# Optimization experiments

Measured on AMD Instinct MI355X. Metric: run time of the kernel, lower is better.

Reference implementation:

```python
import jax, jax.numpy as jnp
import numpy as np

N, F, S, D = 8, 16, 196, 1024
H = 8
HD = D // H
L = 1 + F * S  # global feature token + f*s patch tokens


def _ln(x, g, b, eps=1e-5):
    m = x.mean(-1, keepdims=True)
    v = ((x - m) ** 2).mean(-1, keepdims=True)
    return (x - m) / jnp.sqrt(v + eps) * g + b


def _attn(q, k, v, hd):
    s = jnp.einsum('bqd,bkd->bqk', q, k) / jnp.sqrt(jnp.asarray(hd, q.dtype))
    return jnp.einsum('bqk,bkd->bqd', jax.nn.softmax(s, axis=-1), v)


def setup_inputs() -> dict:
    key = jax.random.key(0)
    ks = jax.random.split(key, 8)
    sc = 0.02
    return {
        'x': jax.random.normal(ks[0], (N, L, D), jnp.float32),
        'W_in': jax.random.normal(ks[1], (D, D), jnp.float32) * sc,
        'b_in': jnp.zeros((D,), jnp.float32),
        'g_in': jnp.ones((D,), jnp.float32),
        'beta_in': jnp.zeros((D,), jnp.float32),
        'W_q': jax.random.normal(ks[2], (D, D), jnp.float32) * sc,
        'W_k': jax.random.normal(ks[3], (D, D), jnp.float32) * sc,
        'W_v': jax.random.normal(ks[4], (D, D), jnp.float32) * sc,
        'g_out': jnp.ones((D,), jnp.float32),
        'beta_out': jnp.zeros((D,), jnp.float32),
        'W_out': jax.random.normal(ks[5], (D, D), jnp.float32) * sc,
        'b_out': jnp.zeros((D,), jnp.float32),
        'att_type': 1,  # 1 == 'time', 0 == 'space' (static)
    }


def reference(x, W_in, b_in, g_in, beta_in, W_q, W_k, W_v, g_out, beta_out, W_out, b_out, att_type):
    n = x.shape[0]
    nh = n * H
    # in_fc: Linear + LayerNorm
    x = _ln(x @ W_in + b_in, g_in, beta_in)
    q, k, v = x @ W_q, x @ W_k, x @ W_v

    def split_heads(y):  # [n, L, D] -> [n*h, L, hd]
        return y.reshape(n, L, H, HD).transpose(0, 2, 1, 3).reshape(nh, L, HD)

    q, k, v = map(split_heads, (q, k, v))
    feat_q, q = q[:, :1], q[:, 1:]
    feat_k, k = k[:, :1], k[:, 1:]
    feat_v, v = v[:, :1], v[:, 1:]

    # token_att is computed in the original but never used (dead code):
    # token_att = _attn(feat_q, k, v, HD)

    if att_type == 1:  # time attention: windows of length F per spatial site
        qt = q.reshape(nh, F, S, HD).transpose(0, 2, 1, 3).reshape(nh * S, F, HD)
        kt = k.reshape(nh, F, S, HD).transpose(0, 2, 1, 3).reshape(nh * S, F, HD)
        vt = v.reshape(nh, F, S, HD).transpose(0, 2, 1, 3).reshape(nh * S, F, HD)
        fk = jnp.tile(feat_k, (S, 1, 1))  # torch .repeat(s,1,1)
        fv = jnp.tile(feat_v, (S, 1, 1))
        kk = jnp.concatenate((fk, kt), axis=1)  # [nh*s, 1+f, hd]
        vv = jnp.concatenate((fv, vt), axis=1)
        seq = _attn(qt, kk, vv, HD)  # [nh*s, f, hd]
        seq = seq.reshape(nh, S, F, HD).transpose(0, 2, 1, 3).reshape(nh, F * S, HD)
    else:  # space attention: windows of length S per frame
        qs = q.reshape(nh * F, S, HD)
        ks_ = k.reshape(nh * F, S, HD)
        vs = v.reshape(nh * F, S, HD)
        fk = jnp.tile(feat_k, (F, 1, 1))
        fv = jnp.tile(feat_v, (F, 1, 1))
        kk = jnp.concatenate((fk, ks_), axis=1)  # [nh*f, 1+s, hd]
        vv = jnp.concatenate((fv, vs), axis=1)
        seq = _attn(qs, kk, vv, HD)  # [nh*f, s, hd]
        seq = seq.reshape(nh, F * S, HD)

    out = jnp.concatenate((feat_q, seq), axis=1)  # [nh, L, hd]
    out = out.reshape(n, H, L, HD).transpose(0, 2, 1, 3).reshape(n, L, D)
    out = _ln(out, g_out, beta_out) @ W_out + b_out
    return out
```

## Files before the change

### kernel.cpp

```cpp
#include <hip/hip_runtime.h>
#include <stdint.h>

#define N_B 8
#define F_T 16
#define S_T 196
#define D_M 1024
#define H_N 8
#define HD  128
#define L_T 3137
#define M_R (N_B * L_T)
#define M_P 25216

typedef __attribute__((ext_vector_type(8))) short bf16x8;
typedef __attribute__((ext_vector_type(4))) float f32x4;

__device__ __forceinline__ float b2f(unsigned int u) {
  union { unsigned int i; float f; } x; x.i = u << 16; return x.f;
}
__device__ __forceinline__ unsigned short f2b(float f) {
  union { float f; unsigned int i; } x; x.f = f;
  unsigned int r = x.i + 0x7fffu + ((x.i >> 16) & 1u);
  return (unsigned short)(r >> 16);
}

__global__ __launch_bounds__(256) void convert_pad(const float* __restrict__ x,
                                                   unsigned short* __restrict__ xb,
                                                   int nreal) {
  int i = (blockIdx.x * 256 + threadIdx.x) * 4;
  float4 v;
  if (i < nreal) v = *(const float4*)(x + i);
  else { v.x = 0.f; v.y = 0.f; v.z = 0.f; v.w = 0.f; }
  ushort4 o;
  o.x = f2b(v.x); o.y = f2b(v.y); o.z = f2b(v.z); o.w = f2b(v.w);
  *(ushort4*)(xb + i) = o;
}

struct WP { const float* s[5]; unsigned short* d[5]; };
__global__ __launch_bounds__(256) void transpose5(WP p) {
  __shared__ float t[32][33];
  const int w = blockIdx.z;
  const float* W = p.s[w];
  unsigned short* Wt = p.d[w];
  const int tx = threadIdx.x, ty = threadIdx.y;
  const int n0 = blockIdx.x * 32, k0 = blockIdx.y * 32;
#pragma unroll
  for (int i = 0; i < 4; i++)
    t[ty + i * 8][tx] = W[(size_t)(k0 + ty + i * 8) * D_M + n0 + tx];
  __syncthreads();
#pragma unroll
  for (int i = 0; i < 4; i++)
    Wt[(size_t)(n0 + ty + i * 8) * D_M + k0 + tx] = f2b(t[tx][ty + i * 8]);
}

__device__ __forceinline__ void async16(const unsigned short* g, unsigned short* l) {
  __builtin_amdgcn_global_load_lds((const __attribute__((address_space(1))) void*)g,
                                   (__attribute__((address_space(3))) void*)l, 16, 0, 0);
}

struct Outs { void* p[3]; };

#define MFMA_Q(AV, MLO)                                                        \
  __builtin_amdgcn_s_setprio(1);                                               \
  _Pragma("unroll") for (int m_ = 0; m_ < 4; ++m_)                             \
      _Pragma("unroll") for (int n_ = 0; n_ < 4; ++n_)                         \
          acc[(MLO) + m_][n_] = __builtin_amdgcn_mfma_f32_16x16x32_bf16(       \
              AV[(MLO) + m_], bv[n_], acc[(MLO) + m_][n_], 0, 0, 0);           \
  __builtin_amdgcn_s_setprio(0);

#define TILE_ONE(T, BUF, STGB, STGA, VMN)                                      \
  do {                                                                         \
    const unsigned short* Ab = sA + (BUF) * 16384 + aOff;                      \
    const unsigned short* Bb = sB + (BUF) * 16384 + bOff;                      \
    if (STGB) {                                                                \
      async16(gB + ((T) + 1) * 64,          sBst + (1 - (BUF)) * 16384);       \
      async16(gB + ((T) + 1) * 64 + 65536,  sBst + (1 - (BUF)) * 16384 + 4096);\
    }                                                                          \
    _Pragma("unroll") for (int m_ = 0; m_ < 4; ++m_)                           \
        av0[m_] = *(const bf16x8*)(Ab + m_ * 1024 + sl0);                      \
    _Pragma("unroll") for (int n_ = 0; n_ < 4; ++n_)                           \
        bv[n_] = *(const bf16x8*)(Bb + n_ * 1024 + sl0);                       \
    _Pragma("unroll") for (int m_ = 0; m_ < 4; ++m_)                           \
        av1[m_] = *(const bf16x8*)(Ab + m_ * 1024 + sl1);                      \
    MFMA_Q(av0, 0)                                                             \
    if (STGB) {                                                                \
      async16(gB + ((T) + 1) * 64 + 131072, sBst + (1 - (BUF)) * 16384 + 8192);\
      async16(gB + ((T) + 1) * 64 + 196608, sBst + (1 - (BUF)) * 16384 + 12288);\
    }                                                                          \
    _Pragma("unroll") for (int m_ = 0; m_ < 4; ++m_)                           \
        av0[4 + m_] = *(const bf16x8*)(Ab + (4 + m_) * 1024 + sl0);            \
    _Pragma("unroll") for (int m_ = 0; m_ < 4; ++m_)                           \
        av1[4 + m_] = *(const bf16x8*)(Ab + (4 + m_) * 1024 + sl1);            \
    MFMA_Q(av0, 4)                                                             \
    asm volatile("s_waitcnt lgkmcnt(0)" ::: "memory");                         \
    __builtin_amdgcn_s_barrier();                                              \
    asm volatile("" ::: "memory");                                             \
    if (STGA) {                                                                \
      async16(gA + ((T) + 2) * 64,          sAst + (BUF) * 16384);             \
      async16(gA + ((T) + 2) * 64 + 65536,  sAst + (BUF) * 16384 + 4096);      \
    }                                                                          \
    _Pragma("unroll") for (int n_ = 0; n_ < 4; ++n_)                           \
        bv[n_] = *(const bf16x8*)(Bb + n_ * 1024 + sl1);                       \
    MFMA_Q(av1, 0)                                                             \
    if (STGA) {                                                                \
      async16(gA + ((T) + 2) * 64 + 131072, sAst + (BUF) * 16384 + 8192);      \
      async16(gA + ((T) + 2) * 64 + 196608, sAst + (BUF) * 16384 + 12288);     \
    }                                                                          \
    MFMA_Q(av1, 4)                                                             \
    if ((VMN) == 4)                                                            \
      asm volatile("s_waitcnt vmcnt(4) lgkmcnt(0)" ::: "memory");              \
    else if ((VMN) == 0)                                                       \
      asm volatile("s_waitcnt vmcnt(0) lgkmcnt(0)" ::: "memory");              \
    else                                                                       \
      asm volatile("s_waitcnt lgkmcnt(0)" ::: "memory");                       \
    __builtin_amdgcn_s_barrier();                                              \
    asm volatile("" ::: "memory");                                             \
  } while (0)

template <int MODE>
__global__ __launch_bounds__(512, 2) void gemm_bt(const unsigned short* __restrict__ A,
                                                  const unsigned short* __restrict__ Bt,
                                                  const float* __restrict__ bias,
                                                  Outs o, int Mreal) {
  __shared__ __align__(16) unsigned short lds[65536];
  unsigned short* sA = lds;
  unsigned short* sB = lds + 32768;

  const int tid = threadIdx.x;
  const int lane = tid & 63;
  const int wv = tid >> 6;
  const int wm = wv >> 2, wn = wv & 3;
  const int l15 = lane & 15, kg = lane >> 4;

  constexpr int NCT = (MODE == 3) ? 12 : 4;
  constexpr int NWG = 99 * NCT;
  constexpr int Q8 = NWG >> 3, R8 = NWG & 7;
  const int xcd = blockIdx.x & 7, off = blockIdx.x >> 3;
  const int lin = (xcd < R8 ? xcd * (Q8 + 1) : R8 * (Q8 + 1) + (xcd - R8) * Q8) + off;
  const int band = lin / 396;
  const int rem = lin - band * 396;
  const int rowBase = (rem >> 2) * 256;
  const int colBase = (band * 4 + (rem & 3)) * 256;

  const int srow = lane >> 3;
  const int gk = ((lane & 7) ^ srow) * 8;
  const unsigned short* gA = A + (size_t)(rowBase + wv * 8 + srow) * 1024 + gk;
  const unsigned short* gB = Bt + (size_t)(colBase + wv * 8 + srow) * 1024 + gk;
  unsigned short* sAst = sA + wv * 512 + lane * 8;
  unsigned short* sBst = sB + wv * 512 + lane * 8;

  const int aOff = (wm * 128 + l15) * 64;
  const int bOff = (wn * 64 + l15) * 64;
  const int sl0 = ((kg) ^ (l15 & 7)) * 8;
  const int sl1 = ((4 + kg) ^ (l15 & 7)) * 8;

  f32x4 acc[8][4] = {};
  bf16x8 av0[8], av1[8], bv[4];

#pragma unroll
  for (int i = 0; i < 4; i++) async16(gA + i * 65536, sAst + i * 4096);
#pragma unroll
  for (int i = 0; i < 4; i++) async16(gB + i * 65536, sBst + i * 4096);
#pragma unroll
  for (int i = 0; i < 4; i++) async16(gA + i * 65536 + 64, sAst + 16384 + i * 4096);
  asm volatile("s_waitcnt vmcnt(4)" ::: "memory");
  __builtin_amdgcn_s_barrier();
  asm volatile("" ::: "memory");

#pragma unroll 1
  for (int tp = 0; tp < 7; ++tp) {
    const int t0 = tp * 2;
    TILE_ONE(t0, 0, true, true, 4);
    TILE_ONE(t0 + 1, 1, true, true, 4);
  }
  TILE_ONE(14, 0, true, false, 0);
  TILE_ONE(15, 1, false, false, -1);

  __syncthreads();
  if (MODE == 2) {
    float* Cf = (float*)lds;
    float* outF = (float*)o.p[0];
#pragma unroll
    for (int p = 0; p < 2; ++p) {
      if (p) __syncthreads();
      if (wm == p) {
#pragma unroll
        for (int n = 0; n < 4; ++n) {
          const int col = wn * 64 + n * 16 + l15;
          const float bval = bias[colBase + col];
#pragma unroll
          for (int m = 0; m < 8; ++m)
#pragma unroll
            for (int r = 0; r < 4; ++r)
              Cf[(m * 16 + kg * 4 + r) * 256 + col] = acc[m][n][r] + bval;
        }
      }
      __syncthreads();
#pragma unroll
      for (int t2 = 0; t2 < 16; ++t2) {
        const int g = t2 * 512 + tid;
        const int row = g >> 6, ch = g & 63;
        const int grow = rowBase + p * 128 + row;
        if (grow < Mreal)
          *(float4*)(outF + (size_t)grow * 1024 + colBase + ch * 4) =
              *(const float4*)(Cf + row * 256 + ch * 4);
      }
    }
  } else {
    unsigned short* Cs = lds;
#pragma unroll
    for (int n = 0; n < 4; ++n) {
      const int col = wn * 64 + n * 16 + l15;
      const float bval = (MODE == 1) ? bias[colBase + col] : 0.f;
#pragma unroll
      for (int m = 0; m < 8; ++m)
#pragma unroll
        for (int r = 0; r < 4; ++r)
          Cs[(wm * 128 + m * 16 + kg * 4 + r) * 256 + col] = f2b(acc[m][n][r] + bval);
    }
    __syncthreads();
    unsigned short* C;
    int cbase;
    if (MODE == 3) { C = (unsigned short*)o.p[colBase >> 10]; cbase = colBase & 1023; }
    else { C = (unsigned short*)o.p[0]; cbase = colBase; }
#pragma unroll
    for (int t2 = 0; t2 < 16; ++t2) {
      const int g = t2 * 512 + tid;
      const int row = g >> 5, ch = g & 31;
      const int grow = rowBase + row;
      if (grow < Mreal)
        *(uint4*)(C + (size_t)grow * 1024 + cbase + ch * 8) =
            *(const uint4*)(Cs + row * 256 + ch * 8);
    }
  }
}

__global__ __launch_bounds__(256) void ln_kernel(const unsigned short* __restrict__ src,
                                                 const unsigned short* __restrict__ src0,
                                                 const float* __restrict__ g,
                                                 const float* __restrict__ beta,
                                                 unsigned short* __restrict__ out, int Mreal) {
  const int row = blockIdx.x, tid = threadIdx.x;
  unsigned short* op = out + (size_t)row * 1024 + tid * 4;
  if (row >= Mreal) {
    ushort4 z; z.x = 0; z.y = 0; z.z = 0; z.w = 0;
    *(ushort4*)op = z;
    return;
  }
  const unsigned short* s = src;
  if (src0 != nullptr && (row % L_T) == 0) s = src0;
  const unsigned short* ip = s + (size_t)row * 1024 + tid * 4;
  uint2 raw = *(const uint2*)ip;
  float x0 = b2f(raw.x & 0xffffu), x1 = b2f(raw.x >> 16);
  float x2 = b2f(raw.y & 0xffffu), x3 = b2f(raw.y >> 16);
  float sum = x0 + x1 + x2 + x3;
  float sq = x0 * x0 + x1 * x1 + x2 * x2 + x3 * x3;
#pragma unroll
  for (int off = 32; off > 0; off >>= 1) {
    sum += __shfl_down(sum, off);
    sq += __shfl_down(sq, off);
  }
  __shared__ float red[8];
  if ((tid & 63) == 0) { red[tid >> 6] = sum; red[4 + (tid >> 6)] = sq; }
  __syncthreads();
  const float ts = red[0] + red[1] + red[2] + red[3];
  const float tq = red[4] + red[5] + red[6] + red[7];
  const float mean = ts * (1.f / 1024.f);
  const float var = tq * (1.f / 1024.f) - mean * mean;
  const float rstd = rsqrtf(var + 1e-5f);
  const float4 gv = *(const float4*)(g + tid * 4);
  const float4 bv = *(const float4*)(beta + tid * 4);
  ushort4 o;
  o.x = f2b((x0 - mean) * rstd * gv.x + bv.x);
  o.y = f2b((x1 - mean) * rstd * gv.y + bv.y);
  o.z = f2b((x2 - mean) * rstd * gv.z + bv.z);
  o.w = f2b((x3 - mean) * rstd * gv.w + bv.w);
  *(ushort4*)op = o;
}

#define ATT_T_BLOCKS (64 * 49)
__global__ __launch_bounds__(256) void attn_kernel(const unsigned short* __restrict__ q,
                                                   const unsigned short* __restrict__ k,
                                                   const unsigned short* __restrict__ v,
                                                   unsigned short* __restrict__ out,
                                                   const int* __restrict__ att_type) {
  __shared__ __align__(16) char smem[22528];
  const int tid = threadIdx.x;
  const int bid = blockIdx.x;
  const int at = att_type[0];

  if (at == 1) {
    if (bid >= ATT_T_BLOCKS) return;
    const int lane = tid & 63, wv = tid >> 6;
    const int l15 = lane & 15, kg = lane >> 4;
    const int hb = bid / 49, sb = bid - hb * 49;
    const int s = sb * 4 + wv;
    const int n = hb >> 3, h = hb & 7;
    const int fi = (hb * S_T + s) & 63;
    const size_t frow = (size_t)(fi >> 3) * L_T;
    const int fcol = (fi & 7) * HD;
    const int qbase = n * L_T + 1 + s;
    const int hcol = h * HD;

    unsigned short* Pl = (unsigned short*)(smem + wv * 5632);
    unsigned short* Vl = (unsigned short*)(smem + wv * 5632 + 1024);

    {
      const int dim0 = l15 * 8;
#pragma unroll
      for (int p = 0; p < 5; p++) {
        const int key = p * 4 + kg;
        if (key < 17) {
          const unsigned short* vp = (key == 0)
              ? (v + frow * 1024 + fcol + dim0)
              : (v + (size_t)(qbase + (key - 1) * S_T) * 1024 + hcol + dim0);
          uint4 r = *(const uint4*)vp;
          unsigned int* wp = (unsigned int*)Vl + key * 65 + l15 * 4;
          wp[0] = r.x; wp[1] = r.y; wp[2] = r.z; wp[3] = r.w;
        }
      }
    }

    bf16x8 aq[4], bk0[4], bk1[4];
    {
      const unsigned short* qp = q + (size_t)(qbase + l15 * S_T) * 1024 + hcol + kg * 8;
      const unsigned short* kp = (l15 == 0)
          ? (k + frow * 1024 + fcol + kg * 8)
          : (k + (size_t)(qbase + (l15 - 1) * S_T) * 1024 + hcol + kg * 8);
      const unsigned short* kp1 = k + (size_t)(qbase + 15 * S_T) * 1024 + hcol + kg * 8;
#pragma unroll
      for (int t = 0; t < 4; t++) {
        aq[t] = *(const bf16x8*)(qp + t * 32);
        bk0[t] = *(const bf16x8*)(kp + t * 32);
        if (l15 == 0) bk1[t] = *(const bf16x8*)(kp1 + t * 32);
        else {
          bf16x8 z = {};
          bk1[t] = z;
        }
      }
    }

    f32x4 c0 = {}, c1 = {};
#pragma unroll
    for (int t = 0; t < 4; t++) {
      c0 = __builtin_amdgcn_mfma_f32_16x16x32_bf16(aq[t], bk0[t], c0, 0, 0, 0);
      c1 = __builtin_amdgcn_mfma_f32_16x16x32_bf16(aq[t], bk1[t], c1, 0, 0, 0);
    }

    const float scl = 0.08838834764831845f;
#pragma unroll
    for (int r = 0; r < 4; r++) {
      float v0 = c0[r] * scl;
      float k16 = __shfl(c1[r] * scl, lane & 48);
      float mx = v0;
#pragma unroll
      for (int m = 1; m < 16; m <<= 1) mx = fmaxf(mx, __shfl_xor(mx, m));
      mx = fmaxf(mx, k16);
      float p = __expf(v0 - mx);
      float p16 = __expf(k16 - mx);
      float sum = p;
#pragma unroll
      for (int m = 1; m < 16; m <<= 1) sum += __shfl_xor(sum, m);
      sum += p16;
      const float inv = 1.f / sum;
      const int row = kg * 4 + r;
      Pl[row * 32 + l15] = f2b(p * inv);
      Pl[row * 32 + 16 + l15] = (l15 == 0) ? f2b(p16 * inv) : (unsigned short)0;
    }

    bf16x8 ap = *(const bf16x8*)(Pl + l15 * 32 + kg * 8);
#pragma unroll
    for (int nt = 0; nt < 8; nt++) {
      const int dim = nt * 16 + l15;
      bf16x8 bvv;
#pragma unroll
      for (int j = 0; j < 8; j++) {
        const int key = kg * 8 + j;
        const int kc = (key < 17) ? key : 0;
        unsigned short raw = Vl[kc * 130 + dim];
        bvv[j] = (key < 17) ? (short)raw : (short)0;
      }
      f32x4 z = {};
      f32x4 o = __builtin_amdgcn_mfma_f32_16x16x32_bf16(ap, bvv, z, 0, 0, 0);
#pragma unroll
      for (int r = 0; r < 4; r++) {
        const int qi = kg * 4 + r;
        out[(size_t)(qbase + qi * S_T) * 1024 + hcol + nt * 16 + l15] = f2b(o[r]);
      }
    }
    return;
  }

  float (*qs)[132] = (float (*)[132])smem;
  float (*sc)[212] = (float (*)[212])(smem + 8448);
  const int hb = bid / 208;
  const int rem = bid - hb * 208;
  const int f = rem / 13, qc = rem - f * 13;
  const int n = hb >> 3, h = hb & 7;
  const int fi = (hb * F_T + f) & 63;
  const size_t frow = (size_t)(fi >> 3) * L_T;
  const int fcol = (fi & 7) * HD;
  const int kbase = n * L_T + 1 + f * S_T;
  const int qbase = kbase + qc * 16;
  const int nk = S_T + 1;
  const int nqv = (qc == 12) ? 4 : 16;
  const int hcol = h * HD;

  {
    const int i = tid >> 4, db = (tid & 15) * 8;
    float* dst = &qs[i][db];
    if (i < nqv) {
      const unsigned short* qp = q + (size_t)(qbase + i) * 1024 + hcol + db;
      uint4 r = *(const uint4*)qp;
      dst[0] = b2f(r.x & 0xffffu); dst[1] = b2f(r.x >> 16);
      dst[2] = b2f(r.y & 0xffffu); dst[3] = b2f(r.y >> 16);
      dst[4] = b2f(r.z & 0xffffu); dst[5] = b2f(r.z >> 16);
      dst[6] = b2f(r.w & 0xffffu); dst[7] = b2f(r.w >> 16);
    } else {
#pragma unroll
      for (int u = 0; u < 8; u++) dst[u] = 0.f;
    }
  }
  __syncthreads();

  const int nslot = 16 * nk;
  for (int slot = tid; slot < nslot; slot += 256) {
    const int i = slot / nk, j = slot - i * nk;
    const unsigned short* kp = (j == 0)
        ? (k + frow * 1024 + fcol)
        : (k + (size_t)(kbase + (j - 1)) * 1024 + hcol);
    float acc = 0.f;
#pragma unroll 4
    for (int d = 0; d < 128; d += 8) {
      uint4 r = *(const uint4*)(kp + d);
      acc += qs[i][d + 0] * b2f(r.x & 0xffffu);
      acc += qs[i][d + 1] * b2f(r.x >> 16);
      acc += qs[i][d + 2] * b2f(r.y & 0xffffu);
      acc += qs[i][d + 3] * b2f(r.y >> 16);
      acc += qs[i][d + 4] * b2f(r.z & 0xffffu);
      acc += qs[i][d + 5] * b2f(r.z >> 16);
      acc += qs[i][d + 6] * b2f(r.w & 0xffffu);
      acc += qs[i][d + 7] * b2f(r.w >> 16);
    }
    sc[i][j] = acc * 0.08838834764831845f;
  }
  __syncthreads();

  if (tid < 16) {
    const int i = tid;
    float m = -1e30f;
    for (int j = 0; j < nk; j++) m = fmaxf(m, sc[i][j]);
    float ssum = 0.f;
    for (int j = 0; j < nk; j++) {
      float e = __expf(sc[i][j] - m);
      sc[i][j] = e;
      ssum += e;
    }
    const float inv = 1.f / ssum;
    for (int j = 0; j < nk; j++) sc[i][j] *= inv;
  }
  __syncthreads();

  {
    const int i = tid >> 4, db = (tid & 15) * 8;
    float o[8];
#pragma unroll
    for (int u = 0; u < 8; u++) o[u] = 0.f;
    for (int j = 0; j < nk; j++) {
      const unsigned short* vp = (j == 0)
          ? (v + frow * 1024 + fcol + db)
          : (v + (size_t)(kbase + (j - 1)) * 1024 + hcol + db);
      const float p = sc[i][j];
      uint4 r = *(const uint4*)vp;
      o[0] += p * b2f(r.x & 0xffffu); o[1] += p * b2f(r.x >> 16);
      o[2] += p * b2f(r.y & 0xffffu); o[3] += p * b2f(r.y >> 16);
      o[4] += p * b2f(r.z & 0xffffu); o[5] += p * b2f(r.z >> 16);
      o[6] += p * b2f(r.w & 0xffffu); o[7] += p * b2f(r.w >> 16);
    }
    if (i < nqv) {
      unsigned short* op = out + (size_t)(qbase + i) * 1024 + hcol + db;
      uint4 w;
      w.x = (unsigned)f2b(o[0]) | ((unsigned)f2b(o[1]) << 16);
      w.y = (unsigned)f2b(o[2]) | ((unsigned)f2b(o[3]) << 16);
      w.z = (unsigned)f2b(o[4]) | ((unsigned)f2b(o[5]) << 16);
      w.w = (unsigned)f2b(o[6]) | ((unsigned)f2b(o[7]) << 16);
      *(uint4*)op = w;
    }
  }
}

extern "C" void kernel_launch(void* const* d_in, const int* in_sizes, int n_in,
                              void* d_out, int out_size, void* d_ws, size_t ws_size,
                              hipStream_t stream) {
  const float* x        = (const float*)d_in[0];
  const float* W_in     = (const float*)d_in[1];
  const float* b_in     = (const float*)d_in[2];
  const float* g_in     = (const float*)d_in[3];
  const float* beta_in  = (const float*)d_in[4];
  const float* W_q      = (const float*)d_in[5];
  const float* W_k      = (const float*)d_in[6];
  const float* W_v      = (const float*)d_in[7];
  const float* g_out    = (const float*)d_in[8];
  const float* beta_out = (const float*)d_in[9];
  const float* W_out    = (const float*)d_in[10];
  const float* b_out    = (const float*)d_in[11];
  const int* att_type   = (const int*)d_in[12];
  float* out = (float*)d_out;

  char* ws = (char*)d_ws;
  const size_t MB = (size_t)M_P * 1024 * 2;
  unsigned short* xb = (unsigned short*)(ws + 0 * MB);
  unsigned short* t1 = (unsigned short*)(ws + 1 * MB);
  unsigned short* xh = (unsigned short*)(ws + 2 * MB);
  unsigned short* kb = (unsigned short*)(ws + 3 * MB);
  unsigned short* vb = (unsigned short*)(ws + 4 * MB);
  unsigned short* wt = (unsigned short*)(ws + 5 * MB);
  const size_t WSZ = (size_t)1024 * 1024;
  unsigned short* wt_in  = wt;
  unsigned short* wqkv   = wt + 1 * WSZ;
  unsigned short* wt_out = wt + 4 * WSZ;

  convert_pad<<<M_P, 256, 0, stream>>>(x, xb, M_R * 1024);

  WP wp;
  wp.s[0] = W_in; wp.s[1] = W_q; wp.s[2] = W_k; wp.s[3] = W_v; wp.s[4] = W_out;
  wp.d[0] = wt_in;
  wp.d[1] = wqkv;
  wp.d[2] = wqkv + 1 * WSZ;
  wp.d[3] = wqkv + 2 * WSZ;
  wp.d[4] = wt_out;
  transpose5<<<dim3(32, 32, 5), dim3(32, 8), 0, stream>>>(wp);

  Outs o1; o1.p[0] = t1; o1.p[1] = nullptr; o1.p[2] = nullptr;
  gemm_bt<1><<<396, 512, 0, stream>>>(xb, wt_in, b_in, o1, M_P);
  ln_kernel<<<M_P, 256, 0, stream>>>(t1, nullptr, g_in, beta_in, xh, M_R);

  Outs oq; oq.p[0] = t1; oq.p[1] = kb; oq.p[2] = vb;
  gemm_bt<3><<<1188, 512, 0, stream>>>(xh, wqkv, nullptr, oq, M_P);

  attn_kernel<<<13312, 256, 0, stream>>>(t1, kb, vb, xb, att_type);
  ln_kernel<<<M_P, 256, 0, stream>>>(xb, t1, g_out, beta_out, xh, M_R);

  Outs oo; oo.p[0] = out; oo.p[1] = nullptr; oo.p[2] = nullptr;
  gemm_bt<2><<<396, 512, 0, stream>>>(xh, wt_out, b_out, oo, M_R);
}
```

Before: 539.1 us.

## Use one wave per row in LayerNorm, grid-stride convert, staged attention output stores

LayerNorm now gives each 64-lane wave one row, loaded with 16-byte vectors, and reduces with wave shuffles only, so the shared-memory reduction and barrier go away. The convert kernel becomes a grid-stride loop over 2048 blocks instead of one block per row. In time attention, the PV results are staged through LDS so each lane writes 16-byte vectors instead of scattered 2-byte stores. The V-operand masking for keys 17 and up is dropped, which relies on the P entries for those keys being zero.

```diff
diff --git a/kernel.cpp b/kernel.cpp
--- a/kernel.cpp
+++ b/kernel.cpp
@@ -26,13 +26,17 @@
 __global__ __launch_bounds__(256) void convert_pad(const float* __restrict__ x,
                                                    unsigned short* __restrict__ xb,
                                                    int nreal) {
-  int i = (blockIdx.x * 256 + threadIdx.x) * 4;
-  float4 v;
-  if (i < nreal) v = *(const float4*)(x + i);
-  else { v.x = 0.f; v.y = 0.f; v.z = 0.f; v.w = 0.f; }
-  ushort4 o;
-  o.x = f2b(v.x); o.y = f2b(v.y); o.z = f2b(v.z); o.w = f2b(v.w);
-  *(ushort4*)(xb + i) = o;
+  const int total4 = M_P * 1024 / 4;
+  const int stride = gridDim.x * 256;
+  for (int i = blockIdx.x * 256 + threadIdx.x; i < total4; i += stride) {
+    const int e = i * 4;
+    float4 v;
+    if (e < nreal) v = *(const float4*)(x + e);
+    else { v.x = 0.f; v.y = 0.f; v.z = 0.f; v.w = 0.f; }
+    ushort4 o;
+    o.x = f2b(v.x); o.y = f2b(v.y); o.z = f2b(v.z); o.w = f2b(v.w);
+    *(ushort4*)(xb + e) = o;
+  }
 }
 
 struct WP { const float* s[5]; unsigned short* d[5]; };
@@ -185,13 +189,13 @@
       if (wm == p) {
 #pragma unroll
         for (int n = 0; n < 4; ++n) {
-          const int col = wn * 64 + n * 16 + l15;
-          const float bval = bias[colBase + col];
+          const int col_l = wn * 64 + n * 16 + l15;
+          const float bval = bias[colBase + col_l];
 #pragma unroll
           for (int m = 0; m < 8; ++m)
 #pragma unroll
             for (int r = 0; r < 4; ++r)
-              Cf[(m * 16 + kg * 4 + r) * 256 + col] = acc[m][n][r] + bval;
+              Cf[(m * 16 + kg * 4 + r) * 256 + col_l] = acc[m][n][r] + bval;
         }
       }
       __syncthreads();
@@ -209,13 +213,13 @@
     unsigned short* Cs = lds;
 #pragma unroll
     for (int n = 0; n < 4; ++n) {
-      const int col = wn * 64 + n * 16 + l15;
-      const float bval = (MODE == 1) ? bias[colBase + col] : 0.f;
+      const int col_l = wn * 64 + n * 16 + l15;
+      const float bval = (MODE == 1) ? bias[colBase + col_l] : 0.f;
 #pragma unroll
       for (int m = 0; m < 8; ++m)
 #pragma unroll
         for (int r = 0; r < 4; ++r)
-          Cs[(wm * 128 + m * 16 + kg * 4 + r) * 256 + col] = f2b(acc[m][n][r] + bval);
+          Cs[(wm * 128 + m * 16 + kg * 4 + r) * 256 + col_l] = f2b(acc[m][n][r] + bval);
     }
     __syncthreads();
     unsigned short* C;
@@ -239,42 +243,62 @@
                                                  const float* __restrict__ g,
                                                  const float* __restrict__ beta,
                                                  unsigned short* __restrict__ out, int Mreal) {
-  const int row = blockIdx.x, tid = threadIdx.x;
-  unsigned short* op = out + (size_t)row * 1024 + tid * 4;
+  const int wv = threadIdx.x >> 6, lane = threadIdx.x & 63;
+  const int row = blockIdx.x * 4 + wv;
+  const int c0 = lane * 8;
+  unsigned short* op = out + (size_t)row * 1024 + c0;
   if (row >= Mreal) {
-    ushort4 z; z.x = 0; z.y = 0; z.z = 0; z.w = 0;
-    *(ushort4*)op = z;
+    uint4 z; z.x = 0; z.y = 0; z.z = 0; z.w = 0;
+    *(uint4*)op = z; *(uint4*)(op + 512) = z;
     return;
   }
   const unsigned short* s = src;
   if (src0 != nullptr && (row % L_T) == 0) s = src0;
-  const unsigned short* ip = s + (size_t)row * 1024 + tid * 4;
-  uint2 raw = *(const uint2*)ip;
-  float x0 = b2f(raw.x & 0xffffu), x1 = b2f(raw.x >> 16);
-  float x2 = b2f(raw.y & 0xffffu), x3 = b2f(raw.y >> 16);
-  float sum = x0 + x1 + x2 + x3;
-  float sq = x0 * x0 + x1 * x1 + x2 * x2 + x3 * x3;
+  const unsigned short* ip = s + (size_t)row * 1024 + c0;
+  const uint4 ra = *(const uint4*)ip;
+  const uint4 rb = *(const uint4*)(ip + 512);
+  float xs[16];
+  xs[0] = b2f(ra.x & 0xffffu);  xs[1] = b2f(ra.x >> 16);
+  xs[2] = b2f(ra.y & 0xffffu);  xs[3] = b2f(ra.y >> 16);
+  xs[4] = b2f(ra.z & 0xffffu);  xs[5] = b2f(ra.z >> 16);
+  xs[6] = b2f(ra.w & 0xffffu);  xs[7] = b2f(ra.w >> 16);
+  xs[8] = b2f(rb.x & 0xffffu);  xs[9] = b2f(rb.x >> 16);
+  xs[10] = b2f(rb.y & 0xffffu); xs[11] = b2f(rb.y >> 16);
+  xs[12] = b2f(rb.z & 0xffffu); xs[13] = b2f(rb.z >> 16);
+  xs[14] = b2f(rb.w & 0xffffu); xs[15] = b2f(rb.w >> 16);
+  float sum = 0.f, sq = 0.f;
+#pragma unroll
+  for (int i = 0; i < 16; ++i) { sum += xs[i]; sq += xs[i] * xs[i]; }
 #pragma unroll
   for (int off = 32; off > 0; off >>= 1) {
-    sum += __shfl_down(sum, off);
-    sq += __shfl_down(sq, off);
-  }
-  __shared__ float red[8];
-  if ((tid & 63) == 0) { red[tid >> 6] = sum; red[4 + (tid >> 6)] = sq; }
-  __syncthreads();
-  const float ts = red[0] + red[1] + red[2] + red[3];
-  const float tq = red[4] + red[5] + red[6] + red[7];
-  const float mean = ts * (1.f / 1024.f);
-  const float var = tq * (1.f / 1024.f) - mean * mean;
+    sum += __shfl_xor(sum, off);
+    sq += __shfl_xor(sq, off);
+  }
+  const float mean = sum * (1.f / 1024.f);
+  const float var = sq * (1.f / 1024.f) - mean * mean;
   const float rstd = rsqrtf(var + 1e-5f);
-  const float4 gv = *(const float4*)(g + tid * 4);
-  const float4 bv = *(const float4*)(beta + tid * 4);
-  ushort4 o;
-  o.x = f2b((x0 - mean) * rstd * gv.x + bv.x);
-  o.y = f2b((x1 - mean) * rstd * gv.y + bv.y);
-  o.z = f2b((x2 - mean) * rstd * gv.z + bv.z);
-  o.w = f2b((x3 - mean) * rstd * gv.w + bv.w);
-  *(ushort4*)op = o;
+  const float4 g0 = *(const float4*)(g + c0),        g1 = *(const float4*)(g + c0 + 4);
+  const float4 g2 = *(const float4*)(g + c0 + 512),  g3 = *(const float4*)(g + c0 + 516);
+  const float4 b0 = *(const float4*)(beta + c0),       b1 = *(const float4*)(beta + c0 + 4);
+  const float4 b2 = *(const float4*)(beta + c0 + 512), b3 = *(const float4*)(beta + c0 + 516);
+  float gg[16] = {g0.x, g0.y, g0.z, g0.w, g1.x, g1.y, g1.z, g1.w,
+                  g2.x, g2.y, g2.z, g2.w, g3.x, g3.y, g3.z, g3.w};
+  float bb[16] = {b0.x, b0.y, b0.z, b0.w, b1.x, b1.y, b1.z, b1.w,
+                  b2.x, b2.y, b2.z, b2.w, b3.x, b3.y, b3.z, b3.w};
+  unsigned short ov[16];
+#pragma unroll
+  for (int i = 0; i < 16; ++i) ov[i] = f2b((xs[i] - mean) * rstd * gg[i] + bb[i]);
+  uint4 wa, wb;
+  wa.x = (unsigned)ov[0] | ((unsigned)ov[1] << 16);
+  wa.y = (unsigned)ov[2] | ((unsigned)ov[3] << 16);
+  wa.z = (unsigned)ov[4] | ((unsigned)ov[5] << 16);
+  wa.w = (unsigned)ov[6] | ((unsigned)ov[7] << 16);
+  wb.x = (unsigned)ov[8] | ((unsigned)ov[9] << 16);
+  wb.y = (unsigned)ov[10] | ((unsigned)ov[11] << 16);
+  wb.z = (unsigned)ov[12] | ((unsigned)ov[13] << 16);
+  wb.w = (unsigned)ov[14] | ((unsigned)ov[15] << 16);
+  *(uint4*)op = wa;
+  *(uint4*)(op + 512) = wb;
 }
 
 #define ATT_T_BLOCKS (64 * 49)
@@ -368,6 +392,7 @@
     }
 
     bf16x8 ap = *(const bf16x8*)(Pl + l15 * 32 + kg * 8);
+    f32x4 oo[8];
 #pragma unroll
     for (int nt = 0; nt < 8; nt++) {
       const int dim = nt * 16 + l15;
@@ -376,16 +401,22 @@
       for (int j = 0; j < 8; j++) {
         const int key = kg * 8 + j;
         const int kc = (key < 17) ? key : 0;
-        unsigned short raw = Vl[kc * 130 + dim];
-        bvv[j] = (key < 17) ? (short)raw : (short)0;
+        bvv[j] = (short)Vl[kc * 130 + dim];
       }
       f32x4 z = {};
-      f32x4 o = __builtin_amdgcn_mfma_f32_16x16x32_bf16(ap, bvv, z, 0, 0, 0);
-#pragma unroll
-      for (int r = 0; r < 4; r++) {
-        const int qi = kg * 4 + r;
-        out[(size_t)(qbase + qi * S_T) * 1024 + hcol + nt * 16 + l15] = f2b(o[r]);
-      }
+      oo[nt] = __builtin_amdgcn_mfma_f32_16x16x32_bf16(ap, bvv, z, 0, 0, 0);
+    }
+
+#pragma unroll
+    for (int nt = 0; nt < 8; nt++)
+#pragma unroll
+      for (int r = 0; r < 4; r++)
+        Vl[(kg * 4 + r) * 130 + nt * 16 + l15] = f2b(oo[nt][r]);
+#pragma unroll
+    for (int t = 0; t < 4; t++) {
+      const int row = t * 4 + kg;
+      uint4 w = *(const uint4*)(Vl + row * 130 + l15 * 8);
+      *(uint4*)(out + (size_t)(qbase + row * S_T) * 1024 + hcol + l15 * 8) = w;
     }
     return;
   }
@@ -519,7 +550,7 @@
   unsigned short* wqkv   = wt + 1 * WSZ;
   unsigned short* wt_out = wt + 4 * WSZ;
 
-  convert_pad<<<M_P, 256, 0, stream>>>(x, xb, M_R * 1024);
+  convert_pad<<<2048, 256, 0, stream>>>(x, xb, M_R * 1024);
 
   WP wp;
   wp.s[0] = W_in; wp.s[1] = W_q; wp.s[2] = W_k; wp.s[3] = W_v; wp.s[4] = W_out;
@@ -532,13 +563,13 @@
 
   Outs o1; o1.p[0] = t1; o1.p[1] = nullptr; o1.p[2] = nullptr;
   gemm_bt<1><<<396, 512, 0, stream>>>(xb, wt_in, b_in, o1, M_P);
-  ln_kernel<<<M_P, 256, 0, stream>>>(t1, nullptr, g_in, beta_in, xh, M_R);
+  ln_kernel<<<M_P / 4, 256, 0, stream>>>(t1, nullptr, g_in, beta_in, xh, M_R);
 
   Outs oq; oq.p[0] = t1; oq.p[1] = kb; oq.p[2] = vb;
   gemm_bt<3><<<1188, 512, 0, stream>>>(xh, wqkv, nullptr, oq, M_P);
 
   attn_kernel<<<13312, 256, 0, stream>>>(t1, kb, vb, xb, att_type);
-  ln_kernel<<<M_P, 256, 0, stream>>>(xb, t1, g_out, beta_out, xh, M_R);
+  ln_kernel<<<M_P / 4, 256, 0, stream>>>(xb, t1, g_out, beta_out, xh, M_R);
 
   Outs oo; oo.p[0] = out; oo.p[1] = nullptr; oo.p[2] = nullptr;
   gemm_bt<2><<<396, 512, 0, stream>>>(xh, wt_out, b_out, oo, M_R);
```

Result: no change. 548.7 us (+1.8%).
